# Optimization experiments

Hardware: AMD Instinct MI355X
Metric: run time of the kernel (lower is better)

Reference implementation:

```python
import jax, jax.numpy as jnp
import numpy as np

N = 2_000_000   # total flattened logits (anchors x classes scale)
FG = 256        # number of foreground (targets==1) entries
DELTA = 1.0


def setup_inputs() -> dict:
    key = jax.random.key(0)
    k1, k2 = jax.random.split(key)
    logits = jax.random.normal(k1, (N,), dtype=jnp.float32)
    fg_idx = jax.random.choice(k2, N, shape=(FG,), replace=False)
    targets = jnp.zeros((N,), dtype=jnp.int32).at[fg_idx].set(1)
    return {"logits": logits, "targets": targets, "fg_num": FG}


def _ap_loss(logits, targets, fg_num):
    """Faithful port of AP_loss: returns (loss [1], grad [N]).

    The torch validity filter (targets==0 & logits >= min(fg)-delta) is
    redundant: for invalid bg, (l - fg_i)/(2*delta)+0.5 < 0, so clamp gives 0.
    We therefore mask with (targets==0) over the full array (static shapes).
    """
    bg_mask = (targets == 0).astype(logits.dtype)
    fg_idx = jnp.nonzero(targets == 1, size=fg_num)[0]
    fg_logits = logits[fg_idx]            # [fg]
    order = jnp.argsort(fg_logits)
    sorted_fg = fg_logits[order]          # ascending, matches torch loop order

    inv2d = 1.0 / (2.0 * DELTA)

    def step(carry, f_i):
        max_prec, bg_grad = carry
        tmp1 = jnp.clip((fg_logits - f_i) * inv2d + 0.5, 0.0, 1.0)   # [fg]
        tmp2 = jnp.clip((logits - f_i) * inv2d + 0.5, 0.0, 1.0) * bg_mask  # [N]
        a = jnp.sum(tmp1) + 0.5
        b = jnp.sum(tmp2)
        cur = a / (a + b)
        new_max = jnp.maximum(max_prec, cur)
        scale = jnp.where(max_prec <= cur, 1.0, (1.0 - max_prec) / (1.0 - cur))
        bg_grad = bg_grad + tmp2 * (scale / (a + b))
        return (new_max, bg_grad), new_max

    init = (jnp.zeros((), logits.dtype), jnp.zeros_like(logits))
    (_, bg_grad), prec_sorted = jax.lax.scan(step, init, sorted_fg)

    prec = jnp.zeros((fg_num,), logits.dtype).at[order].set(prec_sorted)
    grad = bg_grad.at[fg_idx].set(-(1.0 - prec))
    denom = max(fg_num, 1)
    grad = grad / denom
    metric = jnp.sum(prec, keepdims=True) / denom   # [1]
    return 1.0 - metric, grad


def reference(logits, targets, fg_num):
    loss, _ = _ap_loss(logits, targets, fg_num)
    return loss
```

## Files before the change

### kernel.cpp

```cpp
#include <hip/hip_runtime.h>

#define FG    256
#define NBIN  1024
#define BINV  32.0f
#define BOFF  512.0f

typedef unsigned long long u64;
typedef unsigned int u32;


__global__ void init_kernel(int* counter, u64* gacc) {
    int tid = threadIdx.x;
    if (tid == 0) *counter = 0;
    gacc[tid] = 0ull;
}

__global__ void __launch_bounds__(1024) hist_kernel(
        const float* __restrict__ logits,
        const int* __restrict__ targets,
        int* __restrict__ counter,
        float* __restrict__ fgraw,
        u64* __restrict__ gacc, int n) {
    __shared__ u32 h[NBIN];
    const int tid = threadIdx.x;
    h[tid] = 0u;
    __syncthreads();

    const int n4 = n >> 2;
    const float4* l4 = (const float4*)logits;
    const int4*   t4 = (const int4*)targets;
    const int stride = gridDim.x * blockDim.x;
    for (int i = blockIdx.x * blockDim.x + tid; i < n4; i += stride) {
        float4 x = l4[i];
        int4   t = t4[i];
        #pragma unroll
        for (int e = 0; e < 4; ++e) {
            float l  = (e == 0) ? x.x : (e == 1) ? x.y : (e == 2) ? x.z : x.w;
            int   tg = (e == 0) ? t.x : (e == 1) ? t.y : (e == 2) ? t.z : t.w;
            float u = fmaf(l, BINV, BOFF);
            u = fminf(fmaxf(u, 0.f), 1023.99f);
            int b = (int)u;
            u32 qoff = (u32)((u - (float)b) * 32.0f);
            atomicAdd(&h[b], (1u << 18) | qoff);
            if (tg == 1) {
                int p = atomicAdd(counter, 1);
                fgraw[p] = l;
            }
        }
    }
    if (blockIdx.x == 0 && tid == 0) {
        for (int i = n4 << 2; i < n; ++i) {
            float l = logits[i];
            float u = fmaf(l, BINV, BOFF);
            u = fminf(fmaxf(u, 0.f), 1023.99f);
            int b = (int)u;
            u32 qoff = (u32)((u - (float)b) * 32.0f);
            atomicAdd(&h[b], (1u << 18) | qoff);
            if (targets[i] == 1) { int p = atomicAdd(counter, 1); fgraw[p] = l; }
        }
    }
    __syncthreads();
    u32 v = h[tid];
    if (v) {
        u64 pk = ((u64)(v >> 18) << 32) | (u64)(v & 0x3FFFFu);
        atomicAdd(&gacc[tid], pk);
    }
}

__global__ void __launch_bounds__(1024) final_kernel(
        const float* __restrict__ fgraw,
        const u64* __restrict__ gacc,
        float* __restrict__ out, int n) {
    __shared__ float rc[NBIN], rs[NBIN];
    __shared__ float pc[NBIN], ps[NBIN];
    __shared__ float sfv[FG], sf[FG];
    __shared__ int   pr[1024];
    __shared__ float pa[1024];
    __shared__ float wc[16], ws[16];
    __shared__ float wm[4], wsum[4];
    const int tid  = threadIdx.x;
    const int lane = tid & 63;
    const int wv   = tid >> 6;

    {
        u64 v = gacc[tid];
        float cnt = (float)(u32)(v >> 32);
        float qs  = (float)(u32)(v & 0xFFFFFFFFull);
        float binlo = ((float)tid - BOFF) * (1.0f / BINV);
        rc[tid] = cnt;
        rs[tid] = fmaf(qs + 0.5f * cnt, 1.0f / 1024.0f, binlo * cnt);
    }
    if (tid < FG) sfv[tid] = fgraw[tid];
    __syncthreads();

    float c = rc[tid], s = rs[tid];
    #pragma unroll
    for (int off = 1; off < 64; off <<= 1) {
        float tc = __shfl_up(c, off, 64), ts = __shfl_up(s, off, 64);
        if (lane >= off) { c += tc; s += ts; }
    }
    if (lane == 63) { wc[wv] = c; ws[wv] = s; }

    {
        int i = tid & 255, ch = tid >> 8;
        float v = sfv[i];
        int r = 0;
        #pragma unroll 8
        for (int j = ch * 64; j < ch * 64 + 64; ++j) {
            float o = sfv[j];
            r += (o < v || (o == v && j < i)) ? 1 : 0;
        }
        pr[tid] = r;
    }
    __syncthreads();

    if (wv == 0 && lane < 16) {
        float cc = wc[lane], ss = ws[lane];
        #pragma unroll
        for (int off = 1; off < 16; off <<= 1) {
            float tc = __shfl_up(cc, off, 64), ts = __shfl_up(ss, off, 64);
            if (lane >= off) { cc += tc; ss += ts; }
        }
        wc[lane] = cc; ws[lane] = ss;
    }
    if (tid < FG) {
        int r = pr[tid] + pr[tid + 256] + pr[tid + 512] + pr[tid + 768];
        sf[r] = sfv[tid];
    }
    __syncthreads();
    if (wv > 0) { c += wc[wv - 1]; s += ws[wv - 1]; }
    pc[tid] = c; ps[tid] = s;

    {
        int i = tid & 255, ch = tid >> 8;
        float fi = sf[i];
        float sum = 0.f;
        #pragma unroll 8
        for (int j = ch * 64; j < ch * 64 + 64; ++j) {
            float v = (sf[j] - fi) * 0.5f + 0.5f;
            sum += fminf(fmaxf(v, 0.f), 1.f);
        }
        pa[tid] = sum;
    }
    __syncthreads();

    float cur = 0.f;
    if (tid < FG) {
        const float fi = sf[tid];
        const float a = 0.5f + pa[tid] + pa[tid + 256] + pa[tid + 512] + pa[tid + 768];
        float C[2], S[2];
        #pragma unroll
        for (int q = 0; q < 2; ++q) {
            float t = (q == 0) ? (fi - 1.0f) : (fi + 1.0f);
            float u = fmaf(t, BINV, BOFF);
            u = fminf(fmaxf(u, 0.f), 1023.99f);
            float kf = floorf(u);
            int   k  = (int)kf;
            float frac = u - kf;
            C[q] = pc[k] + rc[k] * (frac - 1.0f);
            S[q] = ps[k] + rs[k] * (frac - 1.0f);
        }
        const float Cab   = (float)n - C[1];
        const float Cw    = C[1] - C[0];
        const float Sw    = S[1] - S[0];
        const float b_all = Cab + 0.5f * Sw + (0.5f - 0.5f * fi) * Cw;
        const float b_bg  = b_all - (a - 0.5f);
        cur = a / (a + b_bg);
        float m = cur;
        #pragma unroll
        for (int off = 1; off < 64; off <<= 1) {
            float t = __shfl_up(m, off, 64);
            if (lane >= off) m = fmaxf(m, t);
        }
        if (lane == 63) wm[wv] = m;
        pr[tid] = __float_as_int(m);
    }
    __syncthreads();
    if (tid < FG) {
        float m = __int_as_float(pr[tid]);
        float pmax = -1.f;
        for (int w = 0; w < 4; ++w) if (w < wv) pmax = fmaxf(pmax, wm[w]);
        m = fmaxf(m, pmax);
        float v = m;
        #pragma unroll
        for (int off = 32; off; off >>= 1) v += __shfl_down(v, off, 64);
        if (lane == 0) wsum[wv] = v;
    }
    __syncthreads();
    if (tid == 0) {
        float t = (wsum[0] + wsum[1]) + (wsum[2] + wsum[3]);
        out[0] = 1.f - t / (float)FG;
    }
}

extern "C" void kernel_launch(void* const* d_in, const int* in_sizes, int n_in,
                              void* d_out, int out_size, void* d_ws, size_t ws_size,
                              hipStream_t stream) {
    const float* logits  = (const float*)d_in[0];
    const int*   targets = (const int*)d_in[1];
    const int n = in_sizes[0];

    char*  wb      = (char*)d_ws;
    int*   counter = (int*)wb;
    float* fgraw   = (float*)(wb + 256);
    u64*   gacc    = (u64*)(wb + 2048);
    float* out     = (float*)d_out;

    init_kernel<<<1, NBIN, 0, stream>>>(counter, gacc);
    hist_kernel<<<256, 1024, 0, stream>>>(logits, targets, counter, fgraw, gacc, n);
    final_kernel<<<1, NBIN, 0, stream>>>(fgraw, gacc, out, n);
}
```

Measured before the change: 80.14 us.

## Fuse init, histogram and final kernels into one cooperative launch

Merges the three kernels (workspace init, histogram/foreground gather, final AP computation) into a single cooperative kernel that uses grid-wide syncs instead of kernel boundaries. Block 0 zeroes the counters, all blocks build histograms, then block 0 alone computes the loss after a second grid sync. It aims to remove two launch overheads and inter-kernel gaps, at the cost of two grid barriers, atomic loads and stores for cross-block visibility, and much larger shared memory per block, which may limit co-residency.

```diff
diff --git a/kernel.cpp b/kernel.cpp
--- a/kernel.cpp
+++ b/kernel.cpp
@@ -1,4 +1,7 @@
 #include <hip/hip_runtime.h>
+#include <hip/hip_cooperative_groups.h>
+
+namespace cg = cooperative_groups;
 
 #define FG    256
 #define NBIN  1024
@@ -9,28 +12,40 @@
 typedef unsigned int u32;
 
 
-__global__ void init_kernel(int* counter, u64* gacc) {
-    int tid = threadIdx.x;
-    if (tid == 0) *counter = 0;
-    gacc[tid] = 0ull;
-}
-
-__global__ void __launch_bounds__(1024) hist_kernel(
+__global__ void __launch_bounds__(1024) fused_kernel(
         const float* __restrict__ logits,
         const int* __restrict__ targets,
         int* __restrict__ counter,
         float* __restrict__ fgraw,
-        u64* __restrict__ gacc, int n) {
+        u64* __restrict__ gacc,
+        float* __restrict__ out, int n) {
     __shared__ u32 h[NBIN];
+    __shared__ float rc[NBIN], rs[NBIN];
+    __shared__ float pc[NBIN], ps[NBIN];
+    __shared__ float sfv[FG], sf[FG];
+    __shared__ int   pr[1024];
+    __shared__ float pa[1024];
+    __shared__ float wc[16], ws[16];
+    __shared__ float wm[4], wsum[4];
+
+    cg::grid_group grid = cg::this_grid();
     const int tid = threadIdx.x;
+    const int bid = blockIdx.x;
+    const int lane = tid & 63;
+    const int wv   = tid >> 6;
+
+    if (bid == 0) {
+        if (tid == 0) atomicExch(counter, 0);
+        atomicExch(&gacc[tid], 0ull);
+    }
     h[tid] = 0u;
-    __syncthreads();
+    grid.sync();
 
     const int n4 = n >> 2;
     const float4* l4 = (const float4*)logits;
     const int4*   t4 = (const int4*)targets;
     const int stride = gridDim.x * blockDim.x;
-    for (int i = blockIdx.x * blockDim.x + tid; i < n4; i += stride) {
+    for (int i = bid * blockDim.x + tid; i < n4; i += stride) {
         float4 x = l4[i];
         int4   t = t4[i];
         #pragma unroll
@@ -44,11 +59,11 @@
             atomicAdd(&h[b], (1u << 18) | qoff);
             if (tg == 1) {
                 int p = atomicAdd(counter, 1);
-                fgraw[p] = l;
+                atomicExch((u32*)&fgraw[p], __float_as_uint(l));
             }
         }
     }
-    if (blockIdx.x == 0 && tid == 0) {
+    if (bid == 0 && tid == 0) {
         for (int i = n4 << 2; i < n; ++i) {
             float l = logits[i];
             float u = fmaf(l, BINV, BOFF);
@@ -56,41 +71,33 @@
             int b = (int)u;
             u32 qoff = (u32)((u - (float)b) * 32.0f);
             atomicAdd(&h[b], (1u << 18) | qoff);
-            if (targets[i] == 1) { int p = atomicAdd(counter, 1); fgraw[p] = l; }
-        }
-    }
-    __syncthreads();
-    u32 v = h[tid];
-    if (v) {
-        u64 pk = ((u64)(v >> 18) << 32) | (u64)(v & 0x3FFFFu);
-        atomicAdd(&gacc[tid], pk);
-    }
-}
-
-__global__ void __launch_bounds__(1024) final_kernel(
-        const float* __restrict__ fgraw,
-        const u64* __restrict__ gacc,
-        float* __restrict__ out, int n) {
-    __shared__ float rc[NBIN], rs[NBIN];
-    __shared__ float pc[NBIN], ps[NBIN];
-    __shared__ float sfv[FG], sf[FG];
-    __shared__ int   pr[1024];
-    __shared__ float pa[1024];
-    __shared__ float wc[16], ws[16];
-    __shared__ float wm[4], wsum[4];
-    const int tid  = threadIdx.x;
-    const int lane = tid & 63;
-    const int wv   = tid >> 6;
-
-    {
-        u64 v = gacc[tid];
+            if (targets[i] == 1) {
+                int p = atomicAdd(counter, 1);
+                atomicExch((u32*)&fgraw[p], __float_as_uint(l));
+            }
+        }
+    }
+    __syncthreads();
+    {
+        u32 v = h[tid];
+        if (v) {
+            u64 pk = ((u64)(v >> 18) << 32) | (u64)(v & 0x3FFFFu);
+            atomicAdd(&gacc[tid], pk);
+        }
+    }
+    grid.sync();
+
+    if (bid != 0) return;
+
+    {
+        u64 v = atomicAdd(&gacc[tid], 0ull);
         float cnt = (float)(u32)(v >> 32);
         float qs  = (float)(u32)(v & 0xFFFFFFFFull);
         float binlo = ((float)tid - BOFF) * (1.0f / BINV);
         rc[tid] = cnt;
         rs[tid] = fmaf(qs + 0.5f * cnt, 1.0f / 1024.0f, binlo * cnt);
     }
-    if (tid < FG) sfv[tid] = fgraw[tid];
+    if (tid < FG) sfv[tid] = __uint_as_float(atomicAdd((u32*)&fgraw[tid], 0u));
     __syncthreads();
 
     float c = rc[tid], s = rs[tid];
@@ -144,7 +151,6 @@
     }
     __syncthreads();
 
-    float cur = 0.f;
     if (tid < FG) {
         const float fi = sf[tid];
         const float a = 0.5f + pa[tid] + pa[tid + 256] + pa[tid + 512] + pa[tid + 768];
@@ -165,7 +171,7 @@
         const float Sw    = S[1] - S[0];
         const float b_all = Cab + 0.5f * Sw + (0.5f - 0.5f * fi) * Cw;
         const float b_bg  = b_all - (a - 0.5f);
-        cur = a / (a + b_bg);
+        float cur = a / (a + b_bg);
         float m = cur;
         #pragma unroll
         for (int off = 1; off < 64; off <<= 1) {
@@ -198,7 +204,7 @@
                               hipStream_t stream) {
     const float* logits  = (const float*)d_in[0];
     const int*   targets = (const int*)d_in[1];
-    const int n = in_sizes[0];
+    int n = in_sizes[0];
 
     char*  wb      = (char*)d_ws;
     int*   counter = (int*)wb;
@@ -206,7 +212,8 @@
     u64*   gacc    = (u64*)(wb + 2048);
     float* out     = (float*)d_out;
 
-    init_kernel<<<1, NBIN, 0, stream>>>(counter, gacc);
-    hist_kernel<<<256, 1024, 0, stream>>>(logits, targets, counter, fgraw, gacc, n);
-    final_kernel<<<1, NBIN, 0, stream>>>(fgraw, gacc, out, n);
+    void* args[] = { (void*)&logits, (void*)&targets, (void*)&counter,
+                     (void*)&fgraw,  (void*)&gacc,    (void*)&out, (void*)&n };
+    hipLaunchCooperativeKernel((void*)fused_kernel, dim3(256), dim3(1024),
+                               args, 0, stream);
 }
```

New measurement: 130.6 us. 1.63x slower.
